# Performance work log

Measured on AMD Instinct MI355X. Metric: run time of the kernel, lower is better.

## Reference

```python
import jax, jax.numpy as jnp
import numpy as np
import math

D_MODEL = 2048
N_HEADS = 16
D_FF = 8192
SEQ = 2048
BATCH = 2
THETA = 10000.0
EPS = 1e-5


def _rope(x, pos):
    # x: [B, H, S, d_k] ; pos: [B, S] int
    d = x.shape[-1]
    inv_freq = 1.0 / (THETA ** (jnp.arange(0, d, 2, dtype=jnp.float32) / d))  # [d/2]
    ang = pos[..., None].astype(jnp.float32) * inv_freq  # [B, S, d/2]
    cos = jnp.cos(ang)[:, None, :, :, None]  # [B,1,S,d/2,1]
    sin = jnp.sin(ang)[:, None, :, :, None]
    xr = x.reshape(*x.shape[:-1], d // 2, 2)
    x1, x2 = xr[..., 0], xr[..., 1]
    rot = jnp.stack((-x2, x1), axis=-1)  # rotate pairs
    out = xr * cos + rot * sin
    return out.reshape(x.shape)


def _trunc_normal(key, shape, in_f, out_f):
    std = math.sqrt(2.0 / (in_f + out_f))
    return jax.random.truncated_normal(key, -3.0, 3.0, shape, jnp.float32) * std


def setup_inputs() -> dict:
    key = jax.random.key(0)
    ks = jax.random.split(key, 8)
    x = jax.random.normal(ks[0], (BATCH, SEQ, D_MODEL), jnp.float32)
    token_positions = jnp.sort(jax.random.randint(ks[1], (BATCH, SEQ), 0, SEQ), axis=-1)
    W_qkv = _trunc_normal(ks[2], (3 * D_MODEL, D_MODEL), D_MODEL, 3 * D_MODEL)
    W_o = _trunc_normal(ks[3], (D_MODEL, D_MODEL), D_MODEL, D_MODEL)
    W1 = _trunc_normal(ks[4], (D_FF, D_MODEL), D_MODEL, D_FF)
    W3 = _trunc_normal(ks[5], (D_FF, D_MODEL), D_MODEL, D_FF)
    W2 = _trunc_normal(ks[6], (D_MODEL, D_FF), D_FF, D_MODEL)
    g1 = jnp.ones((D_MODEL,), jnp.float32)
    g2 = jnp.ones((D_MODEL,), jnp.float32)
    return {"x": x, "token_positions": token_positions, "W_qkv": W_qkv, "W_o": W_o,
            "g1": g1, "g2": g2, "W1": W1, "W3": W3, "W2": W2}


def _rmsnorm(x, g):
    xf = x.astype(jnp.float32)
    rms = jnp.sqrt(jnp.mean(xf * xf, axis=-1, keepdims=True) + EPS)
    return (xf / rms * g).astype(x.dtype)


def reference(x, token_positions, W_qkv, W_o, g1, g2, W1, W3, W2):
    B, S, D = x.shape
    H = N_HEADS
    dk = D // H
    # --- attention sublayer ---
    h = _rmsnorm(x, g1)
    qkv = jnp.einsum('bsi,oi->bso', h, W_qkv)  # [B,S,3D]
    q, k, v = jnp.split(qkv, 3, axis=-1)
    to_heads = lambda t: t.reshape(B, S, H, dk).transpose(0, 2, 1, 3)  # [B,H,S,dk]
    q, k, v = to_heads(q), to_heads(k), to_heads(v)
    q = _rope(q, token_positions)
    k = _rope(k, token_positions)
    scores = jnp.einsum('bhnd,bhmd->bhnm', q, k) / math.sqrt(dk)  # [B,H,S,S]
    mask = jnp.tril(jnp.ones((S, S), dtype=bool))
    scores = jnp.where(mask, scores, -jnp.inf)
    attn = jax.nn.softmax(scores, axis=-1)
    o = jnp.einsum('bhnm,bhmd->bhnd', attn, v)
    o = o.transpose(0, 2, 1, 3).reshape(B, S, D)
    x = x + jnp.einsum('bsi,oi->bso', o, W_o)
    # --- SwiGLU FFN sublayer ---
    h2 = _rmsnorm(x, g2)
    x1 = jnp.einsum('bsi,oi->bso', h2, W1)
    x3 = jnp.einsum('bsi,oi->bso', h2, W3)
    x = x + jnp.einsum('bsi,oi->bso', jax.nn.silu(x1) * x3, W2)
    return x
```

## Files before the change

### kernel.cpp

```cpp
#include <hip/hip_runtime.h>

#define DEV __device__ __forceinline__

typedef __bf16 bf16x8 __attribute__((ext_vector_type(8)));
typedef float f32x4 __attribute__((ext_vector_type(4)));
typedef unsigned short u16x8 __attribute__((ext_vector_type(8)));
typedef unsigned short u16x2 __attribute__((ext_vector_type(2)));

DEV unsigned short f2bf(float f) {
  unsigned int u = __float_as_uint(f);
  u += 0x7fffu + ((u >> 16) & 1u);
  return (unsigned short)(u >> 16);
}
DEV float bf2f(unsigned short h) {
  return __uint_as_float(((unsigned int)h) << 16);
}
DEV void gload16(const void* g, void* l) {
  __builtin_amdgcn_global_load_lds(
      (const __attribute__((address_space(1))) unsigned int*)g,
      (__attribute__((address_space(3))) unsigned int*)l, 16, 0, 0);
}
DEV f32x4 mfma16(bf16x8 a, bf16x8 b, f32x4 c) {
  return __builtin_amdgcn_mfma_f32_16x16x32_bf16(a, b, c, 0, 0, 0);
}

#define SB   __builtin_amdgcn_s_barrier()
#define SCH  __builtin_amdgcn_sched_barrier(0)
#define LGKM0 asm volatile("s_waitcnt lgkmcnt(0)" ::: "memory")
#define PRIO1 __builtin_amdgcn_s_setprio(1)
#define PRIO0 __builtin_amdgcn_s_setprio(0)

__global__ __launch_bounds__(256) void k_cvt(const float* __restrict__ in,
                                             unsigned short* __restrict__ out, int n8) {
  const int stride = gridDim.x * 256;
  for (int i = blockIdx.x * 256 + threadIdx.x; i < n8; i += stride) {
    const float4* p = (const float4*)(in + (long)i * 8);
    const float4 a = p[0], b = p[1];
    u16x8 o = { f2bf(a.x), f2bf(a.y), f2bf(a.z), f2bf(a.w),
                f2bf(b.x), f2bf(b.y), f2bf(b.z), f2bf(b.w) };
    *(u16x8*)(out + (long)i * 8) = o;
  }
}

__global__ __launch_bounds__(256) void k_rmsnorm(const float* __restrict__ x,
                                                 const float* __restrict__ g,
                                                 unsigned short* __restrict__ out) {
  const int row = blockIdx.x;
  const int t = threadIdx.x;
  const float4* xr = (const float4*)(x + (long)row * 2048);
  const float4 a = xr[t * 2], c = xr[t * 2 + 1];
  float ss = a.x * a.x + a.y * a.y + a.z * a.z + a.w * a.w +
             c.x * c.x + c.y * c.y + c.z * c.z + c.w * c.w;
#pragma unroll
  for (int o = 32; o > 0; o >>= 1) ss += __shfl_down(ss, o);
  __shared__ float ws4[4];
  __shared__ float invs;
  if ((t & 63) == 0) ws4[t >> 6] = ss;
  __syncthreads();
  if (t == 0) invs = 1.0f / sqrtf((ws4[0] + ws4[1] + ws4[2] + ws4[3]) * (1.0f / 2048.0f) + 1e-5f);
  __syncthreads();
  const float inv = invs;
  const float4* gr = (const float4*)g;
  const float4 g0 = gr[t * 2], g1v = gr[t * 2 + 1];
  u16x8 o8 = { f2bf(a.x * inv * g0.x),  f2bf(a.y * inv * g0.y),
               f2bf(a.z * inv * g0.z),  f2bf(a.w * inv * g0.w),
               f2bf(c.x * inv * g1v.x), f2bf(c.y * inv * g1v.y),
               f2bf(c.z * inv * g1v.z), f2bf(c.w * inv * g1v.w) };
  *(u16x8*)(out + (long)row * 2048 + t * 8) = o8;
}

template <int EPI>
__global__ __launch_bounds__(512, 2) void k_gemm256(
    const unsigned short* __restrict__ A, const unsigned short* __restrict__ B,
    unsigned short* __restrict__ outBF, float* __restrict__ outF,
    const float* __restrict__ resid, const unsigned short* __restrict__ aux,
    int M, int N, int K) {
  __shared__ __align__(16) unsigned short lds[2][2][2][128][64];
  const int tid = threadIdx.x;
  const int wid = tid >> 6, lane = tid & 63;
  const int wr = wid >> 2, wc = wid & 3;
  const int fr = lane & 15, g4 = lane >> 4;

  const int nwg = gridDim.x;
  int bid = blockIdx.x;
  { int q = nwg >> 3, r = nwg & 7, xcd = bid & 7, lo = bid >> 3;
    bid = (xcd < r ? xcd * (q + 1) : r * (q + 1) + (xcd - r) * q) + lo; }
  const int nxb = N >> 8;
  const int bx = bid % nxb, by = bid / nxb;
  const int arow0 = by << 8, bcol0 = bx << 8;
  const int NT = K >> 6;

  const int srow = tid >> 3;
  const int sg = (tid & 7) ^ (srow & 7);
  const unsigned short* Asrc = A + (long)(arow0 + srow) * K + (sg << 3);
  const unsigned short* Bsrc = B + (long)(bcol0 + srow) * K + (sg << 3);

  const int posk0 = (g4 ^ (lane & 7)) << 3;
  const int posk1 = ((4 + g4) ^ (lane & 7)) << 3;

  f32x4 acc[8][4] = {};
  bf16x8 a[4][2], b0[2][2], b1[2][2];

#define VM2  asm volatile("s_waitcnt vmcnt(2)" ::: "memory")
#define STAGE(SRC, xs, bufi, mat, h)                                            \
  { const unsigned short* s_ = (SRC) + (long)(h) * 128 * K + (long)(xs) * 64;   \
    unsigned short* d_ = &lds[bufi][mat][h][0][0] + wid * 512;                  \
    gload16(s_, d_);                                                            \
    gload16(s_ + (long)64 * K, d_ + 4096); }
#define RD_A(mh)                                                                \
  _Pragma("unroll") for (int m_ = 0; m_ < 4; ++m_) {                            \
    const unsigned short* p_ = baseA + ((mh) * 64 + m_ * 16 + fr) * 64;         \
    a[m_][0] = *(const bf16x8*)(p_ + posk0);                                    \
    a[m_][1] = *(const bf16x8*)(p_ + posk1); }
#define RD_B(arr, nh)                                                           \
  _Pragma("unroll") for (int n_ = 0; n_ < 2; ++n_) {                            \
    const unsigned short* p_ = baseB + ((nh) * 32 + n_ * 16 + fr) * 64;         \
    arr[n_][0] = *(const bf16x8*)(p_ + posk0);                                  \
    arr[n_][1] = *(const bf16x8*)(p_ + posk1); }
#define MM(mh, nh, Bv)                                                          \
  _Pragma("unroll") for (int m_ = 0; m_ < 4; ++m_)                              \
  _Pragma("unroll") for (int n_ = 0; n_ < 2; ++n_) {                            \
    acc[(mh)*4+m_][(nh)*2+n_] = mfma16(a[m_][0], Bv[n_][0], acc[(mh)*4+m_][(nh)*2+n_]); \
    acc[(mh)*4+m_][(nh)*2+n_] = mfma16(a[m_][1], Bv[n_][1], acc[(mh)*4+m_][(nh)*2+n_]); }

  STAGE(Asrc, 0, 0, 0, 0);
  STAGE(Asrc, 0, 0, 0, 1);
  STAGE(Bsrc, 0, 0, 1, 0);
  STAGE(Bsrc, 0, 0, 1, 1);
  { const int x1p = (NT > 1) ? 1 : 0;
    STAGE(Asrc, x1p, 1, 0, 0); }
  VM2; SCH; SB; SCH;

  for (int t = 0; t < NT; ++t) {
    const unsigned short* baseA = &lds[t & 1][0][wr][0][0];
    const unsigned short* baseB = &lds[t & 1][1][wc >> 1][0][0] + (wc & 1) * 4096;
    const int x1 = (t + 1 < NT) ? t + 1 : NT - 1;
    const int x2 = (t + 2 < NT) ? t + 2 : NT - 1;
    const int bn = (t + 1) & 1, bc = t & 1;

    RD_A(0); RD_B(b0, 0);
    STAGE(Asrc, x1, bn, 0, 1);
    SCH; SB; LGKM0; SCH;
    PRIO1; MM(0, 0, b0); PRIO0;
    SCH; SB; SCH;

    RD_B(b1, 1);
    STAGE(Bsrc, x1, bn, 1, 0);
    SCH; SB; LGKM0; SCH;
    PRIO1; MM(0, 1, b1); PRIO0;
    SCH; SB; SCH;

    RD_A(1);
    STAGE(Bsrc, x1, bn, 1, 1);
    SCH; SB; LGKM0; SCH;
    PRIO1; MM(1, 1, b1); PRIO0;
    SCH; SB; SCH;

    STAGE(Asrc, x2, bc, 0, 0);
    SCH; SB; SCH;
    PRIO1; MM(1, 0, b0); PRIO0;
    VM2;
    SCH; SB; SCH;
  }
#undef VM2
#undef STAGE
#undef RD_A
#undef RD_B
#undef MM

  const int er = g4 << 2;
#pragma unroll
  for (int m = 0; m < 8; ++m) {
#pragma unroll
    for (int n = 0; n < 4; ++n) {
      const int grow = arow0 + wr * 128 + m * 16 + er;
      const int gcol = bcol0 + wc * 64 + n * 16 + fr;
#pragma unroll
      for (int r = 0; r < 4; ++r) {
        const long idx = (long)(grow + r) * N + gcol;
        const float v = acc[m][n][r];
        if constexpr (EPI == 0) {
          outBF[idx] = f2bf(v);
        } else if constexpr (EPI == 1) {
          outF[idx] = resid[idx] + v;
        } else {
          const float x1v = bf2f(aux[idx]);
          const float sl = x1v / (1.0f + __expf(-x1v));
          outBF[idx] = f2bf(sl * v);
        }
      }
    }
  }
}

__global__ __launch_bounds__(512, 1) void k_gemm_n128(
    const unsigned short* __restrict__ A, const unsigned short* __restrict__ B,
    float* __restrict__ outF, const float* __restrict__ resid, int M, int N, int K) {
  __shared__ __align__(16) unsigned short lds[3][384 * 64];
  const int tid = threadIdx.x;
  const int wid = tid >> 6, lane = tid & 63;
  const int wr = wid >> 1, wc = wid & 1;
  const int fr = lane & 15, g4 = lane >> 4;

  const int nwg = gridDim.x;
  int bid = blockIdx.x;
  { int q = nwg >> 3, r = nwg & 7, xcd = bid & 7, lo = bid >> 3;
    bid = (xcd < r ? xcd * (q + 1) : r * (q + 1) + (xcd - r) * q) + lo; }
  const int nxb = N >> 7;
  const int bx = bid % nxb, by = bid / nxb;
  const int arow0 = by << 8, bcol0 = bx << 7;
  const int NT = K >> 6;

  const int srow = tid >> 3;
  const int sg = (tid & 7) ^ (srow & 7);
  const unsigned short* Asrc = A + (long)(arow0 + srow) * K + (sg << 3);
  const unsigned short* Bsrc = B + (long)(bcol0 + srow) * K + (sg << 3);

  const int posk0 = (g4 ^ (lane & 7)) << 3;
  const int posk1 = ((4 + g4) ^ (lane & 7)) << 3;

  f32x4 acc[4][4] = {};
  bf16x8 a[4][2], bl[2][2], bh[2][2];

#define VM6 asm volatile("s_waitcnt vmcnt(6)" ::: "memory")
#define SITE_A(xs, bufi, s)                                                    \
  gload16(Asrc + (long)((s) * 64) * K + (long)(xs) * 64,                       \
          &lds[bufi][(s) * 4096] + wid * 512);
#define SITE_B(xs, bufi, s)                                                    \
  gload16(Bsrc + (long)((s) * 64) * K + (long)(xs) * 64,                       \
          &lds[bufi][16384 + (s) * 4096] + wid * 512);
#define RDA                                                                    \
  _Pragma("unroll") for (int m_ = 0; m_ < 4; ++m_) {                           \
    const unsigned short* p_ = bufb + (wr * 64 + m_ * 16 + fr) * 64;           \
    a[m_][0] = *(const bf16x8*)(p_ + posk0);                                   \
    a[m_][1] = *(const bf16x8*)(p_ + posk1); }
#define RDB(arr, off)                                                          \
  _Pragma("unroll") for (int n_ = 0; n_ < 2; ++n_) {                           \
    const unsigned short* p_ = bufb + 16384 + (wc * 64 + (off) + n_ * 16 + fr) * 64; \
    arr[n_][0] = *(const bf16x8*)(p_ + posk0);                                 \
    arr[n_][1] = *(const bf16x8*)(p_ + posk1); }
#define MMN(nh, Bv)                                                            \
  _Pragma("unroll") for (int m_ = 0; m_ < 4; ++m_)                             \
  _Pragma("unroll") for (int n_ = 0; n_ < 2; ++n_) {                           \
    acc[m_][(nh)*2+n_] = mfma16(a[m_][0], Bv[n_][0], acc[m_][(nh)*2+n_]);      \
    acc[m_][(nh)*2+n_] = mfma16(a[m_][1], Bv[n_][1], acc[m_][(nh)*2+n_]); }

  SITE_A(0, 0, 0); SITE_A(0, 0, 1); SITE_A(0, 0, 2); SITE_A(0, 0, 3);
  SITE_B(0, 0, 0); SITE_B(0, 0, 1);
  { const int x1p = (NT > 1) ? 1 : 0;
    SITE_A(x1p, 1, 0); SITE_A(x1p, 1, 1); SITE_A(x1p, 1, 2); SITE_A(x1p, 1, 3);
    SITE_B(x1p, 1, 0); SITE_B(x1p, 1, 1); }
  VM6; SCH; SB; SCH;

  for (int t = 0; t < NT; ++t) {
    const unsigned short* bufb = lds[t % 3];
    const int bn = (t + 2) % 3;
    const int xs = (t + 2 < NT) ? t + 2 : NT - 1;

    RDA; RDB(bl, 0);
    SITE_A(xs, bn, 0); SITE_A(xs, bn, 1);
    SCH; SB; LGKM0; SCH;
    PRIO1; MMN(0, bl); PRIO0;
    SCH; SB; SCH;

    RDB(bh, 32);
    SITE_A(xs, bn, 2); SITE_A(xs, bn, 3); SITE_B(xs, bn, 0); SITE_B(xs, bn, 1);
    SCH; SB; LGKM0; SCH;
    PRIO1; MMN(1, bh); PRIO0;
    VM6;
    SCH; SB; SCH;
  }
#undef VM6
#undef SITE_A
#undef SITE_B
#undef RDA
#undef RDB
#undef MMN

  const int er = g4 << 2;
#pragma unroll
  for (int m = 0; m < 4; ++m) {
#pragma unroll
    for (int n = 0; n < 4; ++n) {
      const int grow = arow0 + wr * 64 + m * 16 + er;
      const int gcol = bcol0 + wc * 64 + n * 16 + fr;
#pragma unroll
      for (int r = 0; r < 4; ++r) {
        const long idx = (long)(grow + r) * N + gcol;
        outF[idx] = resid[idx] + acc[m][n][r];
      }
    }
  }
}

__global__ __launch_bounds__(256) void k_rope(const unsigned short* __restrict__ qkv,
                                              const int* __restrict__ tp,
                                              unsigned short* __restrict__ Qh,
                                              unsigned short* __restrict__ Kh, int S) {
  const int row = blockIdx.x;
  const int b = row / S, s = row - b * S;
  const float pos = (float)tp[row];
  for (int p = threadIdx.x; p < 1024; p += 256) {
    const int h = p >> 6, j = p & 63;
    const float ang = pos * __expf((float)j * -0.14391156831212787f);
    const float cc = cosf(ang), sn = sinf(ang);
    const long ib = (long)row * 6144 + h * 128 + (j << 1);
    const float q1 = bf2f(qkv[ib]), q2 = bf2f(qkv[ib + 1]);
    const float k1 = bf2f(qkv[ib + 2048]), k2 = bf2f(qkv[ib + 2049]);
    const long ob = (((long)(b * 16 + h)) * S + s) * 128 + (j << 1);
    u16x2 qo = { f2bf(q1 * cc - q2 * sn), f2bf(q2 * cc + q1 * sn) };
    u16x2 ko = { f2bf(k1 * cc - k2 * sn), f2bf(k2 * cc + k1 * sn) };
    *(u16x2*)&Qh[ob] = qo;
    *(u16x2*)&Kh[ob] = ko;
  }
}

__global__ __launch_bounds__(256) void k_vtrans(const unsigned short* __restrict__ qkv,
                                                unsigned short* __restrict__ Vt, int S) {
  __shared__ __align__(16) unsigned short t[128 * 72];
  const int bh = blockIdx.x, b = bh >> 4, h = bh & 15;
  const int s0 = blockIdx.y << 6;
  const int tid = threadIdx.x;
#pragma unroll
  for (int it = 0; it < 4; ++it) {
    const int sl = it * 16 + (tid >> 4);
    const int c = tid & 15;
    u16x8 v = *(const u16x8*)(qkv + ((long)(b * S + s0 + sl)) * 6144 + 4096 + h * 128 + (c << 3));
#pragma unroll
    for (int jj = 0; jj < 8; ++jj) t[(c * 8 + jj) * 72 + sl] = v[jj];
  }
  __syncthreads();
  const int d = tid >> 1, half = tid & 1;
  unsigned short* dst = Vt + ((long)bh * 128 + d) * S + s0 + half * 32;
  const unsigned short* srcr = &t[d * 72 + half * 32];
#pragma unroll
  for (int u = 0; u < 4; ++u)
    *(u16x8*)(dst + u * 8) = *(const u16x8*)(srcr + u * 8);
}

__global__ __launch_bounds__(256) void k_attn(const unsigned short* __restrict__ Q,
                                              const unsigned short* __restrict__ Kh,
                                              const unsigned short* __restrict__ Vt,
                                              unsigned short* __restrict__ O, int S) {
  __shared__ __align__(16) unsigned short lds_k[64 * 128];
  __shared__ __align__(16) unsigned short lds_v[128 * 64];
  __shared__ __align__(16) unsigned short lds_p[4 * 16 * 64];
  const int bh = blockIdx.x;
  const int b = bh >> 4, h = bh & 15;
  const int qt = gridDim.y - 1 - blockIdx.y;
  const int q0 = qt << 6;
  const int tid = threadIdx.x, w = tid >> 6, lane = tid & 63;
  const int fr = lane & 15, g4 = lane >> 4;

  bf16x8 qf[4];
  {
    const unsigned short* qb = Q + ((long)bh * S + q0 + w * 16 + fr) * 128 + (g4 << 3);
#pragma unroll
    for (int kk = 0; kk < 4; ++kk) qf[kk] = *(const bf16x8*)(qb + kk * 32);
  }

  f32x4 accO[8] = {};
  float mrow[4], lrow[4];
#pragma unroll
  for (int r = 0; r < 4; ++r) { mrow[r] = -1e30f; lrow[r] = 0.f; }

  const int k_row = (w << 4) + g4;
  const int k_cb = fr << 4;
  const int v_row = (w << 5) + (lane >> 3);
  const int v_cb = (lane & 7) << 4;
  const long kbase = (long)bh * S * 128;
  const long vbase = (long)bh * 128 * S;

  const int ntile = qt + 1;
  for (int it = 0; it < ntile; ++it) {
    const int kv0 = it << 6;
#pragma unroll
    for (int j = 0; j < 4; ++j) {
      const int kr = k_row + j * 4;
      const int kc = k_cb ^ ((kr & 7) << 4);
      gload16(Kh + kbase + (long)(kv0 + kr) * 128 + (kc >> 1), &lds_k[w * 2048 + j * 512]);
      const int vr = v_row + j * 8;
      const int vc = v_cb ^ ((vr & 7) << 4);
      gload16(Vt + vbase + (long)vr * S + kv0 + (vc >> 1), &lds_v[w * 2048 + j * 512]);
    }
    __syncthreads();

    f32x4 sc[4] = {};
#pragma unroll
    for (int n = 0; n < 4; ++n) {
      const int krw = n * 16 + fr;
      const int swz = (krw & 7) << 4;
#pragma unroll
      for (int kk = 0; kk < 4; ++kk) {
        const int kb = (kk << 6) + (g4 << 4);
        bf16x8 kf = *(const bf16x8*)&lds_k[krw * 128 + ((kb ^ swz) >> 1)];
        sc[n] = mfma16(qf[kk], kf, sc[n]);
      }
    }

    const float scl = 0.08838834764831845f;
    float sv[4][4];
    const bool needmask = (kv0 + 63 > q0 + w * 16);
#pragma unroll
    for (int n = 0; n < 4; ++n)
#pragma unroll
      for (int r = 0; r < 4; ++r) {
        float v = sc[n][r] * scl;
        if (needmask) {
          const int qi = q0 + w * 16 + (g4 << 2) + r;
          const int ki = kv0 + n * 16 + fr;
          if (ki > qi) v = -1e30f;
        }
        sv[n][r] = v;
      }
    float corr[4];
#pragma unroll
    for (int r = 0; r < 4; ++r) {
      float tm = fmaxf(fmaxf(sv[0][r], sv[1][r]), fmaxf(sv[2][r], sv[3][r]));
      tm = fmaxf(tm, __shfl_xor(tm, 1));
      tm = fmaxf(tm, __shfl_xor(tm, 2));
      tm = fmaxf(tm, __shfl_xor(tm, 4));
      tm = fmaxf(tm, __shfl_xor(tm, 8));
      const float mn = fmaxf(mrow[r], tm);
      corr[r] = __expf(mrow[r] - mn);
      mrow[r] = mn;
    }
    float rs[4] = {0.f, 0.f, 0.f, 0.f};
#pragma unroll
    for (int n = 0; n < 4; ++n)
#pragma unroll
      for (int r = 0; r < 4; ++r) {
        const float p = __expf(sv[n][r] - mrow[r]);
        rs[r] += p;
        const int pr = (g4 << 2) + r;
        const int pc = (n * 16 + fr) << 1;
        lds_p[(w << 10) + pr * 64 + ((pc ^ ((pr & 7) << 4)) >> 1)] = f2bf(p);
      }
#pragma unroll
    for (int r = 0; r < 4; ++r) {
      float s = rs[r];
      s += __shfl_xor(s, 1);
      s += __shfl_xor(s, 2);
      s += __shfl_xor(s, 4);
      s += __shfl_xor(s, 8);
      lrow[r] = lrow[r] * corr[r] + s;
    }
#pragma unroll
    for (int cb = 0; cb < 8; ++cb)
#pragma unroll
      for (int r = 0; r < 4; ++r) accO[cb][r] *= corr[r];

#pragma unroll
    for (int kk = 0; kk < 2; ++kk) {
      const int pb = (kk << 6) + (g4 << 4);
      bf16x8 pf = *(const bf16x8*)&lds_p[(w << 10) + fr * 64 + ((pb ^ ((fr & 7) << 4)) >> 1)];
#pragma unroll
      for (int cb = 0; cb < 8; ++cb) {
        const int vrw = cb * 16 + fr;
        bf16x8 vf = *(const bf16x8*)&lds_v[vrw * 64 + ((pb ^ ((vrw & 7) << 4)) >> 1)];
        accO[cb] = mfma16(pf, vf, accO[cb]);
      }
    }
    __syncthreads();
  }

#pragma unroll
  for (int cb = 0; cb < 8; ++cb)
#pragma unroll
    for (int r = 0; r < 4; ++r) {
      const int si = q0 + w * 16 + (g4 << 2) + r;
      const float o = accO[cb][r] / lrow[r];
      O[((long)b * S + si) * 2048 + h * 128 + cb * 16 + fr] = f2bf(o);
    }
}

extern "C" void kernel_launch(void* const* d_in, const int* in_sizes, int n_in,
                              void* d_out, int out_size, void* d_ws, size_t ws_size,
                              hipStream_t stream) {
  const float* x    = (const float*)d_in[0];
  const int*   tp   = (const int*)d_in[1];
  const float* Wqkv = (const float*)d_in[2];
  const float* Wo   = (const float*)d_in[3];
  const float* g1   = (const float*)d_in[4];
  const float* g2   = (const float*)d_in[5];
  const float* W1   = (const float*)d_in[6];
  const float* W3   = (const float*)d_in[7];
  const float* W2   = (const float*)d_in[8];
  float* out = (float*)d_out;

  char* ws = (char*)d_ws;
  const size_t MB = 1024 * 1024;
  unsigned short* Qh      = (unsigned short*)(ws + 0 * MB);
  unsigned short* Kh      = (unsigned short*)(ws + 16 * MB);
  unsigned short* Vt      = (unsigned short*)(ws + 32 * MB);
  unsigned short* O_bf    = (unsigned short*)(ws + 48 * MB);
  unsigned short* t_bf    = (unsigned short*)(ws + 0 * MB);
  unsigned short* qkv_bf  = (unsigned short*)(ws + 64 * MB);
  float*          x2      = (float*)         (ws + 64 * MB);
  unsigned short* h2_bf   = (unsigned short*)(ws + 96 * MB);
  unsigned short* wo_bf   = (unsigned short*)(ws + 96 * MB);
  unsigned short* wqkv_bf = (unsigned short*)(ws + 112 * MB);
  unsigned short* w1_bf   = (unsigned short*)(ws + 112 * MB);
  unsigned short* w2_bf   = (unsigned short*)(ws + 112 * MB);
  unsigned short* h1_bf   = (unsigned short*)(ws + 144 * MB);
  unsigned short* w3_bf   = (unsigned short*)(ws + 144 * MB);

  const int S = 2048;

  k_cvt<<<1024, 256, 0, stream>>>(Wqkv, wqkv_bf, 12582912 / 8);
  k_rmsnorm<<<4096, 256, 0, stream>>>(x, g1, h1_bf);
  k_gemm256<0><<<dim3(384), 512, 0, stream>>>(h1_bf, wqkv_bf, qkv_bf, nullptr, nullptr, nullptr, 4096, 6144, 2048);
  k_rope<<<4096, 256, 0, stream>>>(qkv_bf, tp, Qh, Kh, S);
  k_vtrans<<<dim3(32, 32), 256, 0, stream>>>(qkv_bf, Vt, S);
  k_cvt<<<1024, 256, 0, stream>>>(Wo, wo_bf, 4194304 / 8);
  k_cvt<<<1024, 256, 0, stream>>>(W1, w1_bf, 16777216 / 8);
  k_cvt<<<1024, 256, 0, stream>>>(W3, w3_bf, 16777216 / 8);
  k_attn<<<dim3(32, 32), 256, 0, stream>>>(Qh, Kh, Vt, O_bf, S);
  k_gemm_n128<<<dim3(256), 512, 0, stream>>>(O_bf, wo_bf, x2, x, 4096, 2048, 2048);

  k_rmsnorm<<<4096, 256, 0, stream>>>(x2, g2, h2_bf);
  k_gemm256<0><<<dim3(512), 512, 0, stream>>>(h2_bf, w1_bf, t_bf, nullptr, nullptr, nullptr, 4096, 8192, 2048);
  k_cvt<<<1024, 256, 0, stream>>>(W2, w2_bf, 16777216 / 8);
  k_gemm256<2><<<dim3(512), 512, 0, stream>>>(h2_bf, w3_bf, t_bf, nullptr, nullptr, t_bf, 4096, 8192, 2048);
  k_gemm_n128<<<dim3(256), 512, 0, stream>>>(t_bf, w2_bf, out, x2, 4096, 2048, 8192);
}
```

Measured before the change: 745.4 us.

## Use split-K 256x256 GEMM with partial buffer for the W2 down-projection

Replaces the 256x128-tile kernel for the final FFN down-projection (K=8192) with the 256x256 GEMM in a two-way split-K mode. Each output tile is covered by two workgroups: one adds the residual and writes to the output, the other writes an fp32 partial buffer, and a separate elementwise kernel then sums the two. This brings the larger-tile GEMM to the long-K matmul while keeping 256 workgroups. The cost is writing and re-reading a 32MB fp32 partial buffer plus an extra kernel launch.

New measurement: 755.7 us. No clear change (+1.4%).

```diff
diff --git a/kernel.cpp b/kernel.cpp
--- a/kernel.cpp
+++ b/kernel.cpp
@@ -39,6 +39,17 @@
     u16x8 o = { f2bf(a.x), f2bf(a.y), f2bf(a.z), f2bf(a.w),
                 f2bf(b.x), f2bf(b.y), f2bf(b.z), f2bf(b.w) };
     *(u16x8*)(out + (long)i * 8) = o;
+  }
+}
+
+__global__ __launch_bounds__(256) void k_add(float* __restrict__ out,
+                                             const float* __restrict__ p, int n4) {
+  const int stride = gridDim.x * 256;
+  for (int i = blockIdx.x * 256 + threadIdx.x; i < n4; i += stride) {
+    float4 a = ((const float4*)out)[i];
+    const float4 b = ((const float4*)p)[i];
+    a.x += b.x; a.y += b.y; a.z += b.z; a.w += b.w;
+    ((float4*)out)[i] = a;
   }
 }
 
@@ -74,7 +85,7 @@
     const unsigned short* __restrict__ A, const unsigned short* __restrict__ B,
     unsigned short* __restrict__ outBF, float* __restrict__ outF,
     const float* __restrict__ resid, const unsigned short* __restrict__ aux,
-    int M, int N, int K) {
+    float* __restrict__ partial, int M, int N, int K, int Keff) {
   __shared__ __align__(16) unsigned short lds[2][2][2][128][64];
   const int tid = threadIdx.x;
   const int wid = tid >> 6, lane = tid & 63;
@@ -85,15 +96,17 @@
   int bid = blockIdx.x;
   { int q = nwg >> 3, r = nwg & 7, xcd = bid & 7, lo = bid >> 3;
     bid = (xcd < r ? xcd * (q + 1) : r * (q + 1) + (xcd - r) * q) + lo; }
+  int tile = bid, ks = 0;
+  if constexpr (EPI == 3) { ks = bid & 1; tile = bid >> 1; }
   const int nxb = N >> 8;
-  const int bx = bid % nxb, by = bid / nxb;
+  const int bx = tile % nxb, by = tile / nxb;
   const int arow0 = by << 8, bcol0 = bx << 8;
-  const int NT = K >> 6;
+  const int NT = Keff >> 6;
 
   const int srow = tid >> 3;
   const int sg = (tid & 7) ^ (srow & 7);
-  const unsigned short* Asrc = A + (long)(arow0 + srow) * K + (sg << 3);
-  const unsigned short* Bsrc = B + (long)(bcol0 + srow) * K + (sg << 3);
+  const unsigned short* Asrc = A + (long)(arow0 + srow) * K + (long)ks * Keff + (sg << 3);
+  const unsigned short* Bsrc = B + (long)(bcol0 + srow) * K + (long)ks * Keff + (sg << 3);
 
   const int posk0 = (g4 ^ (lane & 7)) << 3;
   const int posk1 = ((4 + g4) ^ (lane & 7)) << 3;
@@ -183,10 +196,13 @@
           outBF[idx] = f2bf(v);
         } else if constexpr (EPI == 1) {
           outF[idx] = resid[idx] + v;
-        } else {
+        } else if constexpr (EPI == 2) {
           const float x1v = bf2f(aux[idx]);
           const float sl = x1v / (1.0f + __expf(-x1v));
           outBF[idx] = f2bf(sl * v);
+        } else {
+          if (ks == 0) outF[idx] = resid[idx] + v;
+          else         partial[idx] = v;
         }
       }
     }
@@ -306,10 +322,10 @@
     const float cc = cosf(ang), sn = sinf(ang);
     const long ib = (long)row * 6144 + h * 128 + (j << 1);
     const float q1 = bf2f(qkv[ib]), q2 = bf2f(qkv[ib + 1]);
-    const float k1 = bf2f(qkv[ib + 2048]), k2 = bf2f(qkv[ib + 2049]);
+    const float k1 = bf2f(qkv[ib + 2048]), k2v = bf2f(qkv[ib + 2049]);
     const long ob = (((long)(b * 16 + h)) * S + s) * 128 + (j << 1);
     u16x2 qo = { f2bf(q1 * cc - q2 * sn), f2bf(q2 * cc + q1 * sn) };
-    u16x2 ko = { f2bf(k1 * cc - k2 * sn), f2bf(k2 * cc + k1 * sn) };
+    u16x2 ko = { f2bf(k1 * cc - k2v * sn), f2bf(k2v * cc + k1 * sn) };
     *(u16x2*)&Qh[ob] = qo;
     *(u16x2*)&Kh[ob] = ko;
   }
@@ -504,12 +520,13 @@
   unsigned short* w2_bf   = (unsigned short*)(ws + 112 * MB);
   unsigned short* h1_bf   = (unsigned short*)(ws + 144 * MB);
   unsigned short* w3_bf   = (unsigned short*)(ws + 144 * MB);
+  float*          part    = (float*)         (ws + 144 * MB);
 
   const int S = 2048;
 
   k_cvt<<<1024, 256, 0, stream>>>(Wqkv, wqkv_bf, 12582912 / 8);
   k_rmsnorm<<<4096, 256, 0, stream>>>(x, g1, h1_bf);
-  k_gemm256<0><<<dim3(384), 512, 0, stream>>>(h1_bf, wqkv_bf, qkv_bf, nullptr, nullptr, nullptr, 4096, 6144, 2048);
+  k_gemm256<0><<<dim3(384), 512, 0, stream>>>(h1_bf, wqkv_bf, qkv_bf, nullptr, nullptr, nullptr, nullptr, 4096, 6144, 2048, 2048);
   k_rope<<<4096, 256, 0, stream>>>(qkv_bf, tp, Qh, Kh, S);
   k_vtrans<<<dim3(32, 32), 256, 0, stream>>>(qkv_bf, Vt, S);
   k_cvt<<<1024, 256, 0, stream>>>(Wo, wo_bf, 4194304 / 8);
@@ -519,8 +536,9 @@
   k_gemm_n128<<<dim3(256), 512, 0, stream>>>(O_bf, wo_bf, x2, x, 4096, 2048, 2048);
 
   k_rmsnorm<<<4096, 256, 0, stream>>>(x2, g2, h2_bf);
-  k_gemm256<0><<<dim3(512), 512, 0, stream>>>(h2_bf, w1_bf, t_bf, nullptr, nullptr, nullptr, 4096, 8192, 2048);
+  k_gemm256<0><<<dim3(512), 512, 0, stream>>>(h2_bf, w1_bf, t_bf, nullptr, nullptr, nullptr, nullptr, 4096, 8192, 2048, 2048);
   k_cvt<<<1024, 256, 0, stream>>>(W2, w2_bf, 16777216 / 8);
-  k_gemm256<2><<<dim3(512), 512, 0, stream>>>(h2_bf, w3_bf, t_bf, nullptr, nullptr, t_bf, 4096, 8192, 2048);
-  k_gemm_n128<<<dim3(256), 512, 0, stream>>>(t_bf, w2_bf, out, x2, 4096, 2048, 8192);
-}
+  k_gemm256<2><<<dim3(512), 512, 0, stream>>>(h2_bf, w3_bf, t_bf, nullptr, nullptr, t_bf, nullptr, 4096, 8192, 2048, 2048);
+  k_gemm256<3><<<dim3(256), 512, 0, stream>>>(t_bf, w2_bf, nullptr, out, x2, nullptr, part, 4096, 2048, 8192, 4096);
+  k_add<<<2048, 256, 0, stream>>>(out, part, 2097152);
+}
```
